# Kernel optimization log

Hardware: AMD Instinct MI355X
Metric: run time of the kernel (lower is better)

## Reference

```python
import jax, jax.numpy as jnp
import numpy as np

B, N, E = 128, 2048, 32768   # events, nodes per history graph, temporal edges per graph
C, TC, H = 4, 4, 2           # channels, time_channels, heads (hardcoded in source)
DH = C // H
L = 2                        # num_layers


def setup_inputs() -> dict:
    key = jax.random.key(0)
    ks = jax.random.split(key, 16)
    return {
        "x": jax.random.normal(ks[0], (B, N, C), jnp.float32),
        "edge_index": jax.random.randint(ks[1], (B, 2, E), 0, N),
        "edge_time": jax.random.uniform(ks[2], (B, E), jnp.float32),
        "timestamp": jax.random.uniform(ks[3], (B,), jnp.float32),
        "src_index": jax.random.randint(ks[4], (B,), 0, N),
        "dst_index": jax.random.randint(ks[5], (B,), 0, N),
        "time_w": jax.random.normal(ks[6], (TC,), jnp.float32),
        "time_b": jax.random.normal(ks[7], (TC,), jnp.float32),
        "Wq": jax.random.normal(ks[8], (L, C, C), jnp.float32) / np.sqrt(C).astype(np.float32),
        "Wk": jax.random.normal(ks[9], (L, C + TC, C), jnp.float32) / np.sqrt(C + TC).astype(np.float32),
        "Wv": jax.random.normal(ks[10], (L, C + TC, C), jnp.float32) / np.sqrt(C + TC).astype(np.float32),
        "Wo": jax.random.normal(ks[11], (L, C, C), jnp.float32) / np.sqrt(C).astype(np.float32),
        "bo": jnp.zeros((L, C), jnp.float32),
        "W_lin": jax.random.normal(ks[12], (2 * C + TC, 2), jnp.float32) / np.sqrt(2 * C + TC).astype(np.float32),
        "b_lin": jnp.zeros((2,), jnp.float32),
    }


def _time_enc(t, w, b):
    # TimeEncoder: cos(t * w + b)  (Bochner-style functional time encoding)
    return jnp.cos(t[..., None] * w + b)


def _encode(x, src, dst, phi, Wq, Wk, Wv, Wo, bo):
    # seg id per edge: (batch, dst node) -> flat segment for segment softmax
    seg = (jnp.arange(B, dtype=dst.dtype)[:, None] * N + dst).reshape(-1)  # [B*E]
    h = x
    for l in range(L):
        h_src = jnp.take_along_axis(h, src[:, :, None], axis=1)            # [B,E,C] gather source feats
        msg = jnp.concatenate([h_src, phi], axis=-1)                       # [B,E,C+TC]
        q = (h @ Wq[l]).reshape(B, N, C)                                   # [B,N,C]
        k = (msg @ Wk[l]).reshape(B, E, H, DH)
        v = (msg @ Wv[l]).reshape(B, E, H, DH)
        q_e = jnp.take_along_axis(q, dst[:, :, None], axis=1).reshape(B, E, H, DH)
        logits = (q_e * k).sum(-1) / np.float32(np.sqrt(DH))               # [B,E,H]
        lf = logits.reshape(B * E, H)
        m = jax.ops.segment_max(lf, seg, num_segments=B * N)               # stable softmax max
        p = jnp.exp(lf - m[seg])
        s = jax.ops.segment_sum(p, seg, num_segments=B * N)
        agg = jax.ops.segment_sum(p[:, :, None] * v.reshape(B * E, H, DH), seg, num_segments=B * N)
        attn = (agg / jnp.where(s == 0, 1.0, s)[:, :, None]).reshape(B, N, C)
        h = jax.nn.relu(h + attn @ Wo[l] + bo[l])                          # residual + out-proj + relu
    return h


def reference(x, edge_index, edge_time, timestamp, src_index, dst_index,
              time_w, time_b, Wq, Wk, Wv, Wo, bo, W_lin, b_lin):
    src, dst = edge_index[:, 0, :], edge_index[:, 1, :]
    dt = timestamp[:, None] - edge_time                                    # [B,E] time deltas vs query time
    phi = _time_enc(dt, time_w, time_b)                                    # [B,E,TC]
    h = _encode(x, src, dst, phi, Wq, Wk, Wv, Wo, bo)                      # [B,N,C]
    bidx = jnp.arange(B)
    src_x = h[bidx, src_index]                                             # [B,C]
    dst_x = h[bidx, dst_index]                                             # [B,C]
    time_x = _time_enc(timestamp, time_w, time_b)                          # [B,TC]
    feats = jnp.concatenate([src_x, dst_x, time_x], axis=-1)               # [B,12]
    return feats @ W_lin + b_lin                                           # [B,2]
```

## Files before the change

### kernel.cpp

```cpp
#include <hip/hip_runtime.h>

namespace {

constexpr int B = 128, N = 2048, E = 32768;
constexpr int LOG2N = 11, LOG2E = 15;
constexpr int QE = E / 4;
constexpr int LOG2QE = 13;

constexpr size_t OFF_H0 = 0;
constexpr size_t OFF_H1 = 4u * 1024 * 1024;
constexpr size_t OFF_S8 = 8u * 1024 * 1024;
constexpr size_t OFF_RP = 40u * 1024 * 1024;

__global__ __launch_bounds__(1024) void sort_kernel(const int* __restrict__ edge_index,
                                                    const float* __restrict__ edge_time,
                                                    const float* __restrict__ timestamp,
                                                    int2* __restrict__ sorted8,
                                                    int* __restrict__ row_ptr) {
  __shared__ int  cnt[N];
  __shared__ int  partial[1024];
  __shared__ int2 rec[QE];
  int blk = blockIdx.x, b = blk >> 2, q = blk & 3, t = threadIdx.x;

  cnt[t] = 0; cnt[t + 1024] = 0;
  __syncthreads();

  const int* src_arr = edge_index + (((size_t)(2 * b)) << LOG2E) + q * QE;
  const int* dst_arr = edge_index + (((size_t)(2 * b + 1)) << LOG2E) + q * QE;
  const float* et    = edge_time + (((size_t)b) << LOG2E) + q * QE;
  float ts = timestamp[b];

  for (int e = t; e < QE; e += 1024) atomicAdd(&cnt[dst_arr[e]], 1);
  __syncthreads();

  int i0 = 2 * t, i1 = 2 * t + 1;
  int l0 = cnt[i0], l1 = cnt[i1];
  int sum = l0 + l1;
  partial[t] = sum;
  __syncthreads();
  for (int d = 1; d < 1024; d <<= 1) {
    int v = (t >= d) ? partial[t - d] : 0;
    __syncthreads();
    partial[t] += v;
    __syncthreads();
  }
  int run = partial[t] - sum;
  int run2 = run + l0;
  int* rp = row_ptr + (size_t)blk * (N + 1);
  rp[i0] = run;
  rp[i1] = run2;
  if (t == 1023) rp[N] = QE;
  cnt[i0] = run;
  cnt[i1] = run2;
  __syncthreads();

  for (int e = t; e < QE; e += 1024) {
    int dst = dst_arr[e];
    int src = src_arr[e];
    float dt = ts - et[e];
    int pos = atomicAdd(&cnt[dst], 1);
    rec[pos] = make_int2(src, __float_as_int(dt));
  }
  __syncthreads();

  const int4* rec4 = (const int4*)rec;
  int4* out4 = (int4*)(sorted8 + (((size_t)blk) << LOG2QE));
#pragma unroll
  for (int i = t; i < QE / 2; i += 1024) out4[i] = rec4[i];
}

__global__ __launch_bounds__(1024) void layer_kernel(const float4* __restrict__ h_in,
                                                     float4* __restrict__ h_out,
                                                     const int* __restrict__ row_ptr,
                                                     const int2* __restrict__ sorted8,
                                                     const float* __restrict__ tw,
                                                     const float* __restrict__ tb,
                                                     const float* __restrict__ Wq,
                                                     const float* __restrict__ Wk,
                                                     const float* __restrict__ Wv,
                                                     const float* __restrict__ Wo,
                                                     const float* __restrict__ bo) {
  __shared__ float4 lh[N];
  int blk = blockIdx.x, b = blk >> 1, half = blk & 1, t = threadIdx.x;

  const float4* hb = h_in + (((size_t)b) << LOG2N);
  lh[t] = hb[t];
  lh[t + 1024] = hb[t + 1024];

  float twf[4], tbf[4], bof[4], wq[16], wof[16], wk[32], wv[32];
#pragma unroll
  for (int j = 0; j < 4; j++) { twf[j] = tw[j]; tbf[j] = tb[j]; bof[j] = bo[j]; }
#pragma unroll
  for (int j = 0; j < 16; j++) { wq[j] = Wq[j]; wof[j] = Wo[j]; }
#pragma unroll
  for (int j = 0; j < 32; j++) { wk[j] = Wk[j]; wv[j] = Wv[j]; }
  __syncthreads();

  int n = half * 1024 + t;
  float4 hn = lh[n];
  float q0 = hn.x * wq[0] + hn.y * wq[4] + hn.z * wq[8]  + hn.w * wq[12];
  float q1 = hn.x * wq[1] + hn.y * wq[5] + hn.z * wq[9]  + hn.w * wq[13];
  float q2 = hn.x * wq[2] + hn.y * wq[6] + hn.z * wq[10] + hn.w * wq[14];
  float q3 = hn.x * wq[3] + hn.y * wq[7] + hn.z * wq[11] + hn.w * wq[15];

  float m0 = -INFINITY, m1 = -INFINITY;
  float s0 = 0.f, s1 = 0.f, a00 = 0.f, a01 = 0.f, a10 = 0.f, a11 = 0.f;
  const float RS2 = 0.70710678118654752f;

#pragma unroll
  for (int q = 0; q < 4; ++q) {
    int qblk = b * 4 + q;
    const int* rp = row_ptr + (size_t)qblk * (N + 1);
    const int2* srt = sorted8 + (((size_t)qblk) << LOG2QE);
    int beg = rp[n], end = rp[n + 1];
    for (int i = beg; i < end; ++i) {
      int2 rc = srt[i];
      float dt = __int_as_float(rc.y);
      float4 hs = lh[rc.x];
      float msg[8];
      msg[0] = hs.x; msg[1] = hs.y; msg[2] = hs.z; msg[3] = hs.w;
#pragma unroll
      for (int j = 0; j < 4; j++) msg[4 + j] = __cosf(dt * twf[j] + tbf[j]);
      float k0 = 0, k1 = 0, k2 = 0, k3 = 0, v0 = 0, v1 = 0, v2 = 0, v3 = 0;
#pragma unroll
      for (int j = 0; j < 8; j++) {
        k0 += msg[j] * wk[j * 4 + 0]; k1 += msg[j] * wk[j * 4 + 1];
        k2 += msg[j] * wk[j * 4 + 2]; k3 += msg[j] * wk[j * 4 + 3];
        v0 += msg[j] * wv[j * 4 + 0]; v1 += msg[j] * wv[j * 4 + 1];
        v2 += msg[j] * wv[j * 4 + 2]; v3 += msg[j] * wv[j * 4 + 3];
      }
      float l0 = (q0 * k0 + q1 * k1) * RS2;
      float l1 = (q2 * k2 + q3 * k3) * RS2;
      float nm0 = fmaxf(m0, l0);
      float sc0 = __expf(m0 - nm0);
      float p0  = __expf(l0 - nm0);
      s0 = s0 * sc0 + p0; a00 = a00 * sc0 + p0 * v0; a01 = a01 * sc0 + p0 * v1; m0 = nm0;
      float nm1 = fmaxf(m1, l1);
      float sc1 = __expf(m1 - nm1);
      float p1  = __expf(l1 - nm1);
      s1 = s1 * sc1 + p1; a10 = a10 * sc1 + p1 * v2; a11 = a11 * sc1 + p1 * v3; m1 = nm1;
    }
  }
  float d0 = (s0 == 0.f) ? 1.f : s0;
  float d1 = (s1 == 0.f) ? 1.f : s1;
  float at0 = a00 / d0, at1 = a01 / d0, at2 = a10 / d1, at3 = a11 / d1;
  float o0 = bof[0] + at0 * wof[0] + at1 * wof[4] + at2 * wof[8]  + at3 * wof[12];
  float o1 = bof[1] + at0 * wof[1] + at1 * wof[5] + at2 * wof[9]  + at3 * wof[13];
  float o2 = bof[2] + at0 * wof[2] + at1 * wof[6] + at2 * wof[10] + at3 * wof[14];
  float o3 = bof[3] + at0 * wof[3] + at1 * wof[7] + at2 * wof[11] + at3 * wof[15];
  h_out[(((size_t)b) << LOG2N) + n] =
      make_float4(fmaxf(hn.x + o0, 0.f), fmaxf(hn.y + o1, 0.f),
                  fmaxf(hn.z + o2, 0.f), fmaxf(hn.w + o3, 0.f));
}

__global__ void final_kernel(const float4* __restrict__ h,
                             const int* __restrict__ src_index, const int* __restrict__ dst_index,
                             const float* __restrict__ timestamp,
                             const float* __restrict__ tw,
                             const float* __restrict__ tb,
                             const float* __restrict__ W_lin,
                             const float* __restrict__ b_lin,
                             float* __restrict__ out) {
  int b = threadIdx.x;
  if (b >= B) return;
  float4 sx = h[(((size_t)b) << LOG2N) + src_index[b]];
  float4 dx = h[(((size_t)b) << LOG2N) + dst_index[b]];
  float ts = timestamp[b];
  float f[12];
  f[0] = sx.x; f[1] = sx.y; f[2] = sx.z; f[3] = sx.w;
  f[4] = dx.x; f[5] = dx.y; f[6] = dx.z; f[7] = dx.w;
#pragma unroll
  for (int j = 0; j < 4; j++) f[8 + j] = __cosf(ts * tw[j] + tb[j]);
#pragma unroll
  for (int c = 0; c < 2; c++) {
    float o = b_lin[c];
#pragma unroll
    for (int j = 0; j < 12; j++) o += f[j] * W_lin[j * 2 + c];
    out[b * 2 + c] = o;
  }
}

}

extern "C" void kernel_launch(void* const* d_in, const int* in_sizes, int n_in,
                              void* d_out, int out_size, void* d_ws, size_t ws_size,
                              hipStream_t stream) {
  (void)in_sizes; (void)n_in; (void)out_size; (void)ws_size;
  const float* x         = (const float*)d_in[0];
  const int*   edge_idx  = (const int*)d_in[1];
  const float* edge_time = (const float*)d_in[2];
  const float* timestamp = (const float*)d_in[3];
  const int*   src_index = (const int*)d_in[4];
  const int*   dst_index = (const int*)d_in[5];
  const float* time_w    = (const float*)d_in[6];
  const float* time_b    = (const float*)d_in[7];
  const float* Wq        = (const float*)d_in[8];
  const float* Wk        = (const float*)d_in[9];
  const float* Wv        = (const float*)d_in[10];
  const float* Wo        = (const float*)d_in[11];
  const float* bo        = (const float*)d_in[12];
  const float* W_lin     = (const float*)d_in[13];
  const float* b_lin     = (const float*)d_in[14];

  char* ws = (char*)d_ws;
  float4* h0      = (float4*)(ws + OFF_H0);
  float4* h1      = (float4*)(ws + OFF_H1);
  int2*   sorted8 = (int2*)(ws + OFF_S8);
  int*    row_ptr = (int*)(ws + OFF_RP);

  sort_kernel<<<4 * B, 1024, 0, stream>>>(edge_idx, edge_time, timestamp, sorted8, row_ptr);

  layer_kernel<<<2 * B, 1024, 0, stream>>>((const float4*)x, h1, row_ptr, sorted8,
                                           time_w, time_b,
                                           Wq + 0 * 16, Wk + 0 * 32, Wv + 0 * 32,
                                           Wo + 0 * 16, bo + 0 * 4);
  layer_kernel<<<2 * B, 1024, 0, stream>>>(h1, h0, row_ptr, sorted8,
                                           time_w, time_b,
                                           Wq + 1 * 16, Wk + 1 * 32, Wv + 1 * 32,
                                           Wo + 1 * 16, bo + 1 * 4);

  final_kernel<<<1, 128, 0, stream>>>(h0, src_index, dst_index, timestamp, time_w, time_b,
                                      W_lin, b_lin, (float*)d_out);
}
```

Measured before the change: 185.6 us.

## Pack edge records to 32-bit with fp16 dt, fold q into Wk, smaller blocks

Each sorted edge record shrinks from 8 bytes to 4, storing a 16-bit source index and dt as fp16, and the row_ptr array becomes a packed begin/degree word per node. The layer kernel precomputes q·Wk per node so each edge computes its logits directly, prefetches the next record, and launches 8 blocks of 256 threads per graph instead of 2 blocks of 1024. This cuts memory traffic and per-edge arithmetic and improves load balance. The cost is that dt loses precision through fp16, each block reloads the full node feature tile into shared memory, and the 16-bit packing depends on the fixed sizes N=2048 and QE=8192.

```diff
diff --git a/kernel.cpp b/kernel.cpp
--- a/kernel.cpp
+++ b/kernel.cpp
@@ -1,41 +1,39 @@
 #include <hip/hip_runtime.h>
+#include <hip/hip_fp16.h>
 
 namespace {
 
 constexpr int B = 128, N = 2048, E = 32768;
 constexpr int LOG2N = 11, LOG2E = 15;
-constexpr int QE = E / 4;
-constexpr int LOG2QE = 13;
-
-constexpr size_t OFF_H0 = 0;
-constexpr size_t OFF_H1 = 4u * 1024 * 1024;
-constexpr size_t OFF_S8 = 8u * 1024 * 1024;
-constexpr size_t OFF_RP = 40u * 1024 * 1024;
+constexpr int QE = 8192;
+
+constexpr size_t OFF_H0  = 0;
+constexpr size_t OFF_H1  = 4u * 1024 * 1024;
+constexpr size_t OFF_SRT = 8u * 1024 * 1024;
+constexpr size_t OFF_SEG = 24u * 1024 * 1024;
 
 __global__ __launch_bounds__(1024) void sort_kernel(const int* __restrict__ edge_index,
                                                     const float* __restrict__ edge_time,
                                                     const float* __restrict__ timestamp,
-                                                    int2* __restrict__ sorted8,
-                                                    int* __restrict__ row_ptr) {
-  __shared__ int  cnt[N];
-  __shared__ int  partial[1024];
-  __shared__ int2 rec[QE];
+                                                    unsigned* __restrict__ sorted,
+                                                    unsigned* __restrict__ seg) {
+  __shared__ int      cnt[N];
+  __shared__ int      partial[1024];
+  __shared__ unsigned rec[QE];
   int blk = blockIdx.x, b = blk >> 2, q = blk & 3, t = threadIdx.x;
+  const int* src_arr = edge_index + ((size_t)(2 * b) << LOG2E) + q * QE;
+  const int* dst_arr = edge_index + ((size_t)(2 * b + 1) << LOG2E) + q * QE;
+  const float* et    = edge_time + ((size_t)b << LOG2E) + q * QE;
+  float ts = timestamp[b];
 
   cnt[t] = 0; cnt[t + 1024] = 0;
   __syncthreads();
 
-  const int* src_arr = edge_index + (((size_t)(2 * b)) << LOG2E) + q * QE;
-  const int* dst_arr = edge_index + (((size_t)(2 * b + 1)) << LOG2E) + q * QE;
-  const float* et    = edge_time + (((size_t)b) << LOG2E) + q * QE;
-  float ts = timestamp[b];
-
   for (int e = t; e < QE; e += 1024) atomicAdd(&cnt[dst_arr[e]], 1);
   __syncthreads();
 
   int i0 = 2 * t, i1 = 2 * t + 1;
-  int l0 = cnt[i0], l1 = cnt[i1];
-  int sum = l0 + l1;
+  int l0 = cnt[i0], l1 = cnt[i1], sum = l0 + l1;
   partial[t] = sum;
   __syncthreads();
   for (int d = 1; d < 1024; d <<= 1) {
@@ -46,46 +44,48 @@
   }
   int run = partial[t] - sum;
   int run2 = run + l0;
-  int* rp = row_ptr + (size_t)blk * (N + 1);
-  rp[i0] = run;
-  rp[i1] = run2;
-  if (t == 1023) rp[N] = QE;
+  unsigned* sg = seg + (size_t)blk * N;
+  sg[i0] = (unsigned)run  | ((unsigned)l0 << 16);
+  sg[i1] = (unsigned)run2 | ((unsigned)l1 << 16);
   cnt[i0] = run;
   cnt[i1] = run2;
   __syncthreads();
 
   for (int e = t; e < QE; e += 1024) {
-    int dst = dst_arr[e];
-    int src = src_arr[e];
+    int dst = dst_arr[e], src = src_arr[e];
     float dt = ts - et[e];
+    unsigned hd = (unsigned)__half_as_ushort(__float2half(dt));
     int pos = atomicAdd(&cnt[dst], 1);
-    rec[pos] = make_int2(src, __float_as_int(dt));
-  }
-  __syncthreads();
-
-  const int4* rec4 = (const int4*)rec;
-  int4* out4 = (int4*)(sorted8 + (((size_t)blk) << LOG2QE));
-#pragma unroll
-  for (int i = t; i < QE / 2; i += 1024) out4[i] = rec4[i];
-}
-
-__global__ __launch_bounds__(1024) void layer_kernel(const float4* __restrict__ h_in,
-                                                     float4* __restrict__ h_out,
-                                                     const int* __restrict__ row_ptr,
-                                                     const int2* __restrict__ sorted8,
-                                                     const float* __restrict__ tw,
-                                                     const float* __restrict__ tb,
-                                                     const float* __restrict__ Wq,
-                                                     const float* __restrict__ Wk,
-                                                     const float* __restrict__ Wv,
-                                                     const float* __restrict__ Wo,
-                                                     const float* __restrict__ bo) {
+    rec[pos] = (unsigned)src | (hd << 16);
+  }
+  __syncthreads();
+
+  const uint4* rec4 = (const uint4*)rec;
+  uint4* out4 = (uint4*)(sorted + ((size_t)blk << 13));
+#pragma unroll
+  for (int i = t; i < QE / 4; i += 1024) out4[i] = rec4[i];
+}
+
+__global__ __launch_bounds__(256) void layer_kernel(const float4* __restrict__ h_in,
+                                                    float4* __restrict__ h_out,
+                                                    const unsigned* __restrict__ seg,
+                                                    const unsigned* __restrict__ sorted,
+                                                    const float* __restrict__ tw,
+                                                    const float* __restrict__ tb,
+                                                    const float* __restrict__ Wq,
+                                                    const float* __restrict__ Wk,
+                                                    const float* __restrict__ Wv,
+                                                    const float* __restrict__ Wo,
+                                                    const float* __restrict__ bo) {
   __shared__ float4 lh[N];
-  int blk = blockIdx.x, b = blk >> 1, half = blk & 1, t = threadIdx.x;
-
-  const float4* hb = h_in + (((size_t)b) << LOG2N);
-  lh[t] = hb[t];
-  lh[t + 1024] = hb[t + 1024];
+  int blk = blockIdx.x, b = blk >> 3, oct = blk & 7, t = threadIdx.x;
+
+  const float4* hb = h_in + ((size_t)b << LOG2N);
+#pragma unroll
+  for (int j = 0; j < 8; j++) {
+    int idx = j * 256 + t;
+    lh[idx] = hb[idx];
+  }
 
   float twf[4], tbf[4], bof[4], wq[16], wof[16], wk[32], wv[32];
 #pragma unroll
@@ -96,41 +96,52 @@
   for (int j = 0; j < 32; j++) { wk[j] = Wk[j]; wv[j] = Wv[j]; }
   __syncthreads();
 
-  int n = half * 1024 + t;
+  int n = (oct << 8) + t;
   float4 hn = lh[n];
   float q0 = hn.x * wq[0] + hn.y * wq[4] + hn.z * wq[8]  + hn.w * wq[12];
   float q1 = hn.x * wq[1] + hn.y * wq[5] + hn.z * wq[9]  + hn.w * wq[13];
   float q2 = hn.x * wq[2] + hn.y * wq[6] + hn.z * wq[10] + hn.w * wq[14];
   float q3 = hn.x * wq[3] + hn.y * wq[7] + hn.z * wq[11] + hn.w * wq[15];
+  const float RS2 = 0.70710678118654752f;
+  float u0[8], u1[8];
+#pragma unroll
+  for (int j = 0; j < 8; j++) {
+    u0[j] = RS2 * (q0 * wk[j * 4 + 0] + q1 * wk[j * 4 + 1]);
+    u1[j] = RS2 * (q2 * wk[j * 4 + 2] + q3 * wk[j * 4 + 3]);
+  }
 
   float m0 = -INFINITY, m1 = -INFINITY;
   float s0 = 0.f, s1 = 0.f, a00 = 0.f, a01 = 0.f, a10 = 0.f, a11 = 0.f;
-  const float RS2 = 0.70710678118654752f;
 
 #pragma unroll
   for (int q = 0; q < 4; ++q) {
-    int qblk = b * 4 + q;
-    const int* rp = row_ptr + (size_t)qblk * (N + 1);
-    const int2* srt = sorted8 + (((size_t)qblk) << LOG2QE);
-    int beg = rp[n], end = rp[n + 1];
-    for (int i = beg; i < end; ++i) {
-      int2 rc = srt[i];
-      float dt = __int_as_float(rc.y);
-      float4 hs = lh[rc.x];
-      float msg[8];
-      msg[0] = hs.x; msg[1] = hs.y; msg[2] = hs.z; msg[3] = hs.w;
-#pragma unroll
-      for (int j = 0; j < 4; j++) msg[4 + j] = __cosf(dt * twf[j] + tbf[j]);
-      float k0 = 0, k1 = 0, k2 = 0, k3 = 0, v0 = 0, v1 = 0, v2 = 0, v3 = 0;
-#pragma unroll
-      for (int j = 0; j < 8; j++) {
-        k0 += msg[j] * wk[j * 4 + 0]; k1 += msg[j] * wk[j * 4 + 1];
-        k2 += msg[j] * wk[j * 4 + 2]; k3 += msg[j] * wk[j * 4 + 3];
-        v0 += msg[j] * wv[j * 4 + 0]; v1 += msg[j] * wv[j * 4 + 1];
-        v2 += msg[j] * wv[j * 4 + 2]; v3 += msg[j] * wv[j * 4 + 3];
-      }
-      float l0 = (q0 * k0 + q1 * k1) * RS2;
-      float l1 = (q2 * k2 + q3 * k3) * RS2;
+    int qblk = (b << 2) + q;
+    unsigned sd = seg[(size_t)qblk * N + n];
+    int beg = (int)(sd & 0xFFFFu);
+    int deg = (int)(sd >> 16);
+    const unsigned* srt = sorted + ((size_t)qblk << 13) + beg;
+    unsigned rc = (deg > 0) ? srt[0] : 0u;
+    for (int j = 0; j < deg; ++j) {
+      unsigned rc_next = (j + 1 < deg) ? srt[j + 1] : 0u;
+      int src = (int)(rc & 0xFFFFu);
+      float dt = __half2float(__ushort_as_half((unsigned short)(rc >> 16)));
+      float4 hs = lh[src];
+      float p0c = __cosf(dt * twf[0] + tbf[0]);
+      float p1c = __cosf(dt * twf[1] + tbf[1]);
+      float p2c = __cosf(dt * twf[2] + tbf[2]);
+      float p3c = __cosf(dt * twf[3] + tbf[3]);
+      float l0 = u0[0] * hs.x + u0[1] * hs.y + u0[2] * hs.z + u0[3] * hs.w
+               + u0[4] * p0c + u0[5] * p1c + u0[6] * p2c + u0[7] * p3c;
+      float l1 = u1[0] * hs.x + u1[1] * hs.y + u1[2] * hs.z + u1[3] * hs.w
+               + u1[4] * p0c + u1[5] * p1c + u1[6] * p2c + u1[7] * p3c;
+      float v0 = wv[0] * hs.x + wv[4] * hs.y + wv[8]  * hs.z + wv[12] * hs.w
+               + wv[16] * p0c + wv[20] * p1c + wv[24] * p2c + wv[28] * p3c;
+      float v1 = wv[1] * hs.x + wv[5] * hs.y + wv[9]  * hs.z + wv[13] * hs.w
+               + wv[17] * p0c + wv[21] * p1c + wv[25] * p2c + wv[29] * p3c;
+      float v2 = wv[2] * hs.x + wv[6] * hs.y + wv[10] * hs.z + wv[14] * hs.w
+               + wv[18] * p0c + wv[22] * p1c + wv[26] * p2c + wv[30] * p3c;
+      float v3 = wv[3] * hs.x + wv[7] * hs.y + wv[11] * hs.z + wv[15] * hs.w
+               + wv[19] * p0c + wv[23] * p1c + wv[27] * p2c + wv[31] * p3c;
       float nm0 = fmaxf(m0, l0);
       float sc0 = __expf(m0 - nm0);
       float p0  = __expf(l0 - nm0);
@@ -139,6 +150,7 @@
       float sc1 = __expf(m1 - nm1);
       float p1  = __expf(l1 - nm1);
       s1 = s1 * sc1 + p1; a10 = a10 * sc1 + p1 * v2; a11 = a11 * sc1 + p1 * v3; m1 = nm1;
+      rc = rc_next;
     }
   }
   float d0 = (s0 == 0.f) ? 1.f : s0;
@@ -148,7 +160,7 @@
   float o1 = bof[1] + at0 * wof[1] + at1 * wof[5] + at2 * wof[9]  + at3 * wof[13];
   float o2 = bof[2] + at0 * wof[2] + at1 * wof[6] + at2 * wof[10] + at3 * wof[14];
   float o3 = bof[3] + at0 * wof[3] + at1 * wof[7] + at2 * wof[11] + at3 * wof[15];
-  h_out[(((size_t)b) << LOG2N) + n] =
+  h_out[((size_t)b << LOG2N) + n] =
       make_float4(fmaxf(hn.x + o0, 0.f), fmaxf(hn.y + o1, 0.f),
                   fmaxf(hn.z + o2, 0.f), fmaxf(hn.w + o3, 0.f));
 }
@@ -203,21 +215,21 @@
   const float* b_lin     = (const float*)d_in[14];
 
   char* ws = (char*)d_ws;
-  float4* h0      = (float4*)(ws + OFF_H0);
-  float4* h1      = (float4*)(ws + OFF_H1);
-  int2*   sorted8 = (int2*)(ws + OFF_S8);
-  int*    row_ptr = (int*)(ws + OFF_RP);
-
-  sort_kernel<<<4 * B, 1024, 0, stream>>>(edge_idx, edge_time, timestamp, sorted8, row_ptr);
-
-  layer_kernel<<<2 * B, 1024, 0, stream>>>((const float4*)x, h1, row_ptr, sorted8,
-                                           time_w, time_b,
-                                           Wq + 0 * 16, Wk + 0 * 32, Wv + 0 * 32,
-                                           Wo + 0 * 16, bo + 0 * 4);
-  layer_kernel<<<2 * B, 1024, 0, stream>>>(h1, h0, row_ptr, sorted8,
-                                           time_w, time_b,
-                                           Wq + 1 * 16, Wk + 1 * 32, Wv + 1 * 32,
-                                           Wo + 1 * 16, bo + 1 * 4);
+  float4*   h0     = (float4*)(ws + OFF_H0);
+  float4*   h1     = (float4*)(ws + OFF_H1);
+  unsigned* sorted = (unsigned*)(ws + OFF_SRT);
+  unsigned* seg    = (unsigned*)(ws + OFF_SEG);
+
+  sort_kernel<<<4 * B, 1024, 0, stream>>>(edge_idx, edge_time, timestamp, sorted, seg);
+
+  layer_kernel<<<8 * B, 256, 0, stream>>>((const float4*)x, h1, seg, sorted,
+                                          time_w, time_b,
+                                          Wq + 0 * 16, Wk + 0 * 32, Wv + 0 * 32,
+                                          Wo + 0 * 16, bo + 0 * 4);
+  layer_kernel<<<8 * B, 256, 0, stream>>>(h1, h0, seg, sorted,
+                                          time_w, time_b,
+                                          Wq + 1 * 16, Wk + 1 * 32, Wv + 1 * 32,
+                                          Wo + 1 * 16, bo + 1 * 4);
 
   final_kernel<<<1, 128, 0, stream>>>(h0, src_index, dst_index, timestamp, time_w, time_b,
                                       W_lin, b_lin, (float*)d_out);
```

New measurement: 195.8 us. 1.05x slower.
